# Optimization experiments

Hardware: AMD Instinct MI355X
Metric: run time of the kernel (lower is better)

Reference implementation:

```python
import jax, jax.numpy as jnp
import numpy as np

EMBED_DIM = 1024
NUM_HEADS = 16
HEAD_DIM = EMBED_DIM // NUM_HEADS
BATCH = 4
SEQ = 2048


def setup_inputs() -> dict:
    key = jax.random.key(0)
    ks = jax.random.split(key, 5)
    s_in = 1.0 / np.sqrt(EMBED_DIM)
    x = jax.random.normal(ks[0], (BATCH, SEQ, EMBED_DIM), dtype=jnp.float32)
    # torch nn.Linear params: weight [out, in], bias [out]
    qkv_w = jax.random.uniform(ks[1], (3 * EMBED_DIM, EMBED_DIM), jnp.float32, -s_in, s_in)
    qkv_b = jax.random.uniform(ks[2], (3 * EMBED_DIM,), jnp.float32, -s_in, s_in)
    out_w = jax.random.uniform(ks[3], (EMBED_DIM, EMBED_DIM), jnp.float32, -s_in, s_in)
    out_b = jax.random.uniform(ks[4], (EMBED_DIM,), jnp.float32, -s_in, s_in)
    return {"x": x, "qkv_w": qkv_w, "qkv_b": qkv_b, "out_w": out_w, "out_b": out_b}


def reference(x, qkv_w, qkv_b, out_w, out_b):
    B, S, E = x.shape
    qkv = x @ qkv_w.T + qkv_b                      # [B,S,3E]
    qkv = qkv.reshape(B, S, 3, NUM_HEADS, HEAD_DIM)
    qkv = jnp.transpose(qkv, (2, 0, 3, 1, 4))      # [3,B,H,S,D]
    q, k, v = qkv[0], qkv[1], qkv[2]
    scale = jnp.sqrt(jnp.float32(HEAD_DIM))
    scores = jnp.einsum('bhqd,bhkd->bhqk', q, k) / scale  # [B,H,S,S]
    attn = jax.nn.softmax(scores, axis=-1)
    out = jnp.einsum('bhqk,bhkd->bhqd', attn, v)   # [B,H,S,D]
    out = jnp.transpose(out, (0, 2, 1, 3)).reshape(B, S, E)
    return out @ out_w.T + out_b
```

## Files before the change

kernel.cpp:

```cpp
#include <hip/hip_runtime.h>
#include <hip/hip_bf16.h>

typedef _Float16 f16;
typedef __attribute__((ext_vector_type(8))) _Float16 f16x8;
typedef __attribute__((ext_vector_type(4))) _Float16 f16x4;
typedef __attribute__((ext_vector_type(4))) float f32x4;

#define MFMA16(a, b, c) __builtin_amdgcn_mfma_f32_16x16x32_f16(a, b, c, 0, 0, 0)
#define GLDS(src, dst) __builtin_amdgcn_global_load_lds( \
    (const __attribute__((address_space(1))) void*)(src), \
    (__attribute__((address_space(3))) void*)(dst), 16, 0, 0)

__device__ inline unsigned pkrtz(float a, float b) {
    __fp16 __attribute__((ext_vector_type(2))) r = __builtin_amdgcn_cvt_pkrtz(a, b);
    unsigned u; __builtin_memcpy(&u, &r, 4);
    return u;
}
__device__ inline void pl32swap(unsigned& a, unsigned& b) {
    asm volatile("v_permlane32_swap_b32 %0, %1" : "+v"(a), "+v"(b));
}
__device__ inline void pl16swap(unsigned& a, unsigned& b) {
    asm volatile("v_permlane16_swap_b32 %0, %1" : "+v"(a), "+v"(b));
}
__device__ inline float fexp2(float x) {
#if __has_builtin(__builtin_amdgcn_exp2f)
    return __builtin_amdgcn_exp2f(x);
#else
    return exp2f(x);
#endif
}

__global__ void cvt_all(const float4* __restrict__ x, const float4* __restrict__ qw,
                        const float4* __restrict__ ow,
                        f16x4* __restrict__ xo, f16x4* __restrict__ qwo,
                        f16x4* __restrict__ owo) {
    const int N1 = 2097152, N2 = 786432, N3 = 262144;
    int i = blockIdx.x * blockDim.x + threadIdx.x;
    int stride = gridDim.x * blockDim.x;
    for (; i < N1 + N2 + N3; i += stride) {
        const float4* src; f16x4* dst; int j;
        if (i < N1)            { src = x;  dst = xo;  j = i; }
        else if (i < N1 + N2)  { src = qw; dst = qwo; j = i - N1; }
        else                   { src = ow; dst = owo; j = i - N1 - N2; }
        float4 f = src[j];
        f16x4 h;
        h.x = (f16)f.x; h.y = (f16)f.y; h.z = (f16)f.z; h.w = (f16)f.w;
        dst[j] = h;
    }
}

__global__ __launch_bounds__(256, 2) void gemm_bt(
    const f16* __restrict__ A, const f16* __restrict__ Bw,
    const float* __restrict__ bias, int mode, int nbn, int chunk,
    f16* __restrict__ qo, f16* __restrict__ ko, f16* __restrict__ vo,
    float* __restrict__ outp)
{
    __shared__ __align__(16) f16 As[128 * 64];
    __shared__ __align__(16) f16 Bs[128 * 64];
    const int bid = blockIdx.x;
    const int vid = (bid & 7) * chunk + (bid >> 3);
    const int brow = (vid / nbn) * 128;
    const int bcol = (vid % nbn) * 128;
    const int tid = threadIdx.x;
    const int wave = tid >> 6, lane = tid & 63;
    const int wr = wave >> 1, wc = wave & 1;
    const int K = 1024;
    const f16* Ab = A + (size_t)brow * K;
    const f16* Bb = Bw + (size_t)bcol * K;

    const f32x4 fz = {0.0f, 0.0f, 0.0f, 0.0f};
    f32x4 acc[4][4];
#pragma unroll
    for (int m = 0; m < 4; ++m)
#pragma unroll
        for (int n = 0; n < 4; ++n) acc[m][n] = fz;

    const int lrow = lane >> 3;
    const int lcol = (lane & 7) * 8;
    const int cl = lane & 15, rg = lane >> 4;

    for (int k0 = 0; k0 < K; k0 += 64) {
        __syncthreads();
#pragma unroll
        for (int c = 0; c < 4; ++c) {
            const int ch = wave * 4 + c;
            GLDS(Ab + (size_t)(ch * 8 + lrow) * K + k0 + lcol, As + ch * 512);
            GLDS(Bb + (size_t)(ch * 8 + lrow) * K + k0 + lcol, Bs + ch * 512);
        }
        __syncthreads();
#pragma unroll
        for (int kk = 0; kk < 2; ++kk) {
            f16x8 af[4], bfr[4];
#pragma unroll
            for (int m = 0; m < 4; ++m)
                af[m] = *(const f16x8*)(As + (wr * 64 + m * 16 + cl) * 64 + kk * 32 + rg * 8);
#pragma unroll
            for (int n = 0; n < 4; ++n)
                bfr[n] = *(const f16x8*)(Bs + (wc * 64 + n * 16 + cl) * 64 + kk * 32 + rg * 8);
#pragma unroll
            for (int m = 0; m < 4; ++m)
#pragma unroll
                for (int n = 0; n < 4; ++n)
                    acc[m][n] = MFMA16(af[m], bfr[n], acc[m][n]);
        }
    }

    if (mode == 0) {
#pragma unroll
        for (int n = 0; n < 4; ++n) {
            int col = bcol + wc * 64 + n * 16 + cl;
            float bs = bias[col];
            int which = col >> 10;
            int h = (col & 1023) >> 6;
            int d = col & 63;
            if (which == 2) {
#pragma unroll
                for (int m = 0; m < 4; ++m) {
                    int row0 = brow + wr * 64 + m * 16 + rg * 4;
                    int bb = row0 >> 11, s0 = row0 & 2047;
                    f16x4 pk;
#pragma unroll
                    for (int r = 0; r < 4; ++r) pk[r] = (f16)(acc[m][n][r] + bs);
                    *(f16x4*)(vo + ((size_t)(bb * 16 + h) * 64 + d) * 2048 + s0) = pk;
                }
            } else {
                f16* dst = (which == 0) ? qo : ko;
                float scale = (which == 0) ? 0.125f * 1.44269504f : 1.0f;
#pragma unroll
                for (int m = 0; m < 4; ++m) {
#pragma unroll
                    for (int r = 0; r < 4; ++r) {
                        int row = brow + wr * 64 + m * 16 + rg * 4 + r;
                        int bb = row >> 11, s = row & 2047;
                        dst[((size_t)(bb * 16 + h) * 2048 + s) * 64 + d] =
                            (f16)((acc[m][n][r] + bs) * scale);
                    }
                }
            }
        }
    } else {
#pragma unroll
        for (int n = 0; n < 4; ++n) {
            int col = bcol + wc * 64 + n * 16 + cl;
            float bs = bias[col];
#pragma unroll
            for (int m = 0; m < 4; ++m)
#pragma unroll
                for (int r = 0; r < 4; ++r) {
                    int row = brow + wr * 64 + m * 16 + rg * 4 + r;
                    outp[(size_t)row * 1024 + col] = acc[m][n][r] + bs;
                }
        }
    }
}

__global__ __launch_bounds__(256, 3) void attn_fwd(
    const f16* __restrict__ Q, const f16* __restrict__ Kg,
    const f16* __restrict__ Vtg, f16* __restrict__ AO)
{
    const int bid = blockIdx.x;
    const int vid = (bid & 7) * 128 + (bid >> 3);
    const int qx = vid & 15;
    const int bh = vid >> 4;
    const int q0 = qx * 128;
    const int tid = threadIdx.x;
    const int wave = tid >> 6, lane = tid & 63;
    const int cl = lane & 15, rg = lane >> 4;
    const f16* Qh = Q + (size_t)bh * 2048 * 64;
    const f16* Kp = Kg + (size_t)bh * 2048 * 64;
    const f16* Vp = Vtg + (size_t)bh * 64 * 2048;

    __shared__ __align__(16) f16 Ks[2][64 * 64];
    __shared__ __align__(16) f16 Vs[2][64 * 64];

    f16x8 aq[2][2];
#pragma unroll
    for (int m = 0; m < 2; ++m) {
        const f16* qptr = Qh + (size_t)(q0 + wave * 32 + m * 16 + cl) * 64 + rg * 8;
        aq[m][0] = *(const f16x8*)(qptr);
        aq[m][1] = *(const f16x8*)(qptr + 32);
    }

    f16x8 ones8;
#pragma unroll
    for (int j = 0; j < 8; ++j) ones8[j] = (f16)1.0f;

    const int srow0 = tid >> 3;
    const int schunk = tid & 7;
    const int swz = cl & 7;

    const f32x4 fz = {0.0f, 0.0f, 0.0f, 0.0f};
    f32x4 oacc[2][4];
    f32x4 loacc[2];
#pragma unroll
    for (int m = 0; m < 2; ++m) {
        loacc[m] = fz;
#pragma unroll
        for (int da = 0; da < 4; ++da) oacc[m][da] = fz;
    }

#pragma unroll
    for (int c = 0; c < 2; ++c) {
        int row = c * 32 + srow0;
        int sc = (schunk ^ (row & 7)) * 8;
        GLDS(Kp + (size_t)row * 64 + sc,   &Ks[0][(c * 256 + wave * 64) * 8]);
        GLDS(Vp + (size_t)row * 2048 + sc, &Vs[0][(c * 256 + wave * 64) * 8]);
    }

    int cur = 0;
    for (int t = 0; t < 32; ++t) {
        if (t < 31) {
            const int kt = (t + 1) * 64;
#pragma unroll
            for (int c = 0; c < 2; ++c) {
                int row = c * 32 + srow0;
                int sc = (schunk ^ (row & 7)) * 8;
                GLDS(Kp + (size_t)(kt + row) * 64 + sc, &Ks[cur ^ 1][(c * 256 + wave * 64) * 8]);
                GLDS(Vp + (size_t)row * 2048 + kt + sc, &Vs[cur ^ 1][(c * 256 + wave * 64) * 8]);
            }
            asm volatile("s_waitcnt vmcnt(4)" ::: "memory");
        } else {
            asm volatile("s_waitcnt vmcnt(0)" ::: "memory");
        }
        __builtin_amdgcn_sched_barrier(0);
        __builtin_amdgcn_s_barrier();
        __builtin_amdgcn_sched_barrier(0);

        f32x4 sacc[2][4];
        __builtin_amdgcn_s_setprio(1);
#pragma unroll
        for (int fn = 0; fn < 4; ++fn) {
            f16x8 ak0 = *(const f16x8*)(
                &Ks[cur][(fn * 16 + cl) * 64 + (rg ^ swz) * 8]);
            f16x8 ak1 = *(const f16x8*)(
                &Ks[cur][(fn * 16 + cl) * 64 + ((4 | rg) ^ swz) * 8]);
            sacc[0][fn] = MFMA16(ak0, aq[0][0], fz);
            sacc[0][fn] = MFMA16(ak1, aq[0][1], sacc[0][fn]);
            sacc[1][fn] = MFMA16(ak0, aq[1][0], fz);
            sacc[1][fn] = MFMA16(ak1, aq[1][1], sacc[1][fn]);
        }
        __builtin_amdgcn_s_setprio(0);

        f16x8 pbv[2][2];
#pragma unroll
        for (int m = 0; m < 2; ++m) {
            unsigned X0[4], X1[4];
#pragma unroll
            for (int fn = 0; fn < 4; ++fn) {
                float p0 = fexp2(sacc[m][fn][0]);
                float p1 = fexp2(sacc[m][fn][1]);
                float p2 = fexp2(sacc[m][fn][2]);
                float p3 = fexp2(sacc[m][fn][3]);
                X0[fn] = pkrtz(p0, p1);
                X1[fn] = pkrtz(p2, p3);
            }
#pragma unroll
            for (int kk = 0; kk < 2; ++kk) {
                unsigned a0 = X0[2 * kk], b0 = X0[2 * kk + 1];
                unsigned a1 = X1[2 * kk], b1 = X1[2 * kk + 1];
                pl32swap(a0, b0); pl16swap(a0, b0);
                pl32swap(a1, b1); pl16swap(a1, b1);
                unsigned fr[4] = {a0, a1, b0, b1};
                __builtin_memcpy(&pbv[m][kk], fr, 16);
            }
        }

        __builtin_amdgcn_s_setprio(1);
#pragma unroll
        for (int kk = 0; kk < 2; ++kk) {
            loacc[0] = MFMA16(ones8, pbv[0][kk], loacc[0]);
            loacc[1] = MFMA16(ones8, pbv[1][kk], loacc[1]);
#pragma unroll
            for (int da = 0; da < 4; ++da) {
                f16x8 av = *(const f16x8*)(
                    &Vs[cur][(da * 16 + cl) * 64 + (((kk << 2) | rg) ^ swz) * 8]);
                oacc[0][da] = MFMA16(av, pbv[0][kk], oacc[0][da]);
                oacc[1][da] = MFMA16(av, pbv[1][kk], oacc[1][da]);
            }
        }
        __builtin_amdgcn_s_setprio(0);

        asm volatile("s_waitcnt lgkmcnt(0)" ::: "memory");
        __builtin_amdgcn_sched_barrier(0);
        __builtin_amdgcn_s_barrier();
        __builtin_amdgcn_sched_barrier(0);
        cur ^= 1;
    }

    const int bb = bh >> 4, h = bh & 15;
#pragma unroll
    for (int m = 0; m < 2; ++m) {
        float inv = 1.0f / loacc[m][0];
        int s = q0 + wave * 32 + m * 16 + cl;
        f16* op = AO + ((size_t)(bb * 2048 + s) * 16 + h) * 64;
#pragma unroll
        for (int da = 0; da < 4; ++da) {
            f16x4 ov;
#pragma unroll
            for (int r = 0; r < 4; ++r) ov[r] = (f16)(oacc[m][da][r] * inv);
            *(f16x4*)(op + da * 16 + rg * 4) = ov;
        }
    }
}

extern "C" void kernel_launch(void* const* d_in, const int* in_sizes, int n_in,
                              void* d_out, int out_size, void* d_ws, size_t ws_size,
                              hipStream_t stream) {
    const float* x     = (const float*)d_in[0];
    const float* qkv_w = (const float*)d_in[1];
    const float* qkv_b = (const float*)d_in[2];
    const float* out_w = (const float*)d_in[3];
    const float* out_b = (const float*)d_in[4];
    float* out = (float*)d_out;

    char* ws = (char*)d_ws;
    size_t off = 0;
    f16* x_h  = (f16*)(ws + off); off += 16777216;
    f16* qw_h = (f16*)(ws + off); off += 6291456;
    f16* ow_h = (f16*)(ws + off); off += 2097152;
    f16* Qb   = (f16*)(ws + off); off += 16777216;
    f16* Kb   = (f16*)(ws + off); off += 16777216;
    f16* Vb   = (f16*)(ws + off); off += 16777216;
    f16* AO   = (f16*)(ws + off); off += 16777216;

    cvt_all<<<2048, 256, 0, stream>>>((const float4*)x, (const float4*)qkv_w,
                                      (const float4*)out_w,
                                      (f16x4*)x_h, (f16x4*)qw_h, (f16x4*)ow_h);

    gemm_bt<<<1536, dim3(256), 0, stream>>>(x_h, qw_h, qkv_b, 0, 24, 192,
                                            Qb, Kb, Vb, nullptr);
    attn_fwd<<<1024, dim3(256), 0, stream>>>(Qb, Kb, Vb, AO);
    gemm_bt<<<512, dim3(256), 0, stream>>>(AO, ow_h, out_b, 1, 8, 64,
                                           nullptr, nullptr, nullptr, out);
}
```

Measured before the change: 189.2 us.

## Add 256x256 double-buffered QKV GEMM kernel with swizzled LDS and phased pipeline

Replaces the generic 128x128 QKV projection GEMM with a dedicated 256x256-tile kernel using 512 threads. It double-buffers LDS, XOR-swizzles the shared-memory layout, and interleaves global-to-LDS loads with MFMA phases under explicit waitcnt, barriers and setprio. The aim is more data reuse per tile and hiding of load latency. The output GEMM becomes its own specialised kernel. The cost is 128 KB of LDS per block and only 384 blocks, which lowers occupancy and risks tail imbalance across CUs.

```diff
diff --git a/kernel.cpp b/kernel.cpp
--- a/kernel.cpp
+++ b/kernel.cpp
@@ -49,18 +49,158 @@
     }
 }
 
-__global__ __launch_bounds__(256, 2) void gemm_bt(
+__global__ __launch_bounds__(512, 2) void gemm256_qkv(
     const f16* __restrict__ A, const f16* __restrict__ Bw,
-    const float* __restrict__ bias, int mode, int nbn, int chunk,
-    f16* __restrict__ qo, f16* __restrict__ ko, f16* __restrict__ vo,
-    float* __restrict__ outp)
+    const float* __restrict__ bias,
+    f16* __restrict__ qo, f16* __restrict__ ko, f16* __restrict__ vo)
+{
+    __shared__ __align__(16) f16 As[2][16384];
+    __shared__ __align__(16) f16 Bs[2][16384];
+    const int tid = threadIdx.x;
+    const int wave = tid >> 6, lane = tid & 63;
+    const int wr = wave >> 2, wc = wave & 3;
+    const int bid = blockIdx.x;
+    const int vid = (bid & 7) * 48 + (bid >> 3);
+    const int brow = (vid / 12) * 256;
+    const int bcol = (vid % 12) * 256;
+    const f16* Ab = A + (size_t)brow * 1024;
+    const f16* Bb = Bw + (size_t)bcol * 1024;
+
+    const int cl = lane & 15, rg = lane >> 4;
+    const int swz = cl & 7;
+    const int strow = tid >> 3;
+    const int ssc = ((tid & 7) ^ (strow & 7)) * 8;
+
+#define STG_A(db, s, kcol) GLDS(Ab + (size_t)((s) * 64 + strow) * 1024 + (kcol) + ssc, \
+                                &As[db][(s) * 4096 + wave * 512])
+#define STG_B(db, s, kcol) GLDS(Bb + (size_t)((s) * 64 + strow) * 1024 + (kcol) + ssc, \
+                                &Bs[db][(s) * 4096 + wave * 512])
+
+    const f32x4 fz = {0.0f, 0.0f, 0.0f, 0.0f};
+    f32x4 acc[8][4];
+#pragma unroll
+    for (int m = 0; m < 8; ++m)
+#pragma unroll
+        for (int n = 0; n < 4; ++n) acc[m][n] = fz;
+    f16x8 bf[4][2];
+
+#pragma unroll
+    for (int s = 0; s < 4; ++s) STG_A(0, s, 0);
+#pragma unroll
+    for (int s = 0; s < 4; ++s) STG_B(0, s, 0);
+#pragma unroll
+    for (int s = 0; s < 4; ++s) STG_B(1, s, 64);
+    STG_A(1, 0, 64); STG_A(1, 2, 64);
+    asm volatile("s_waitcnt vmcnt(6)" ::: "memory");
+    __builtin_amdgcn_sched_barrier(0);
+    __builtin_amdgcn_s_barrier();
+    __builtin_amdgcn_sched_barrier(0);
+
+#define PHASE(BUF, Q, BW, ...)                                                   \
+    do {                                                                         \
+        f16x8 af[2][2];                                                          \
+        _Pragma("unroll")                                                        \
+        for (int mi = 0; mi < 2; ++mi)                                           \
+            _Pragma("unroll")                                                    \
+            for (int kk = 0; kk < 2; ++kk)                                       \
+                af[mi][kk] = *(const f16x8*)(&As[BUF][(wr * 2 + ((Q) >> 1)) * 4096 \
+                    + (((Q) & 1) * 32 + mi * 16 + cl) * 64                       \
+                    + (((kk << 2) | rg) ^ swz) * 8]);                            \
+        if ((Q) == 0) {                                                          \
+            _Pragma("unroll")                                                    \
+            for (int n = 0; n < 4; ++n)                                          \
+                _Pragma("unroll")                                                \
+                for (int kk = 0; kk < 2; ++kk)                                   \
+                    bf[n][kk] = *(const f16x8*)(&Bs[BUF][wc * 4096               \
+                        + (n * 16 + cl) * 64 + (((kk << 2) | rg) ^ swz) * 8]);   \
+        }                                                                        \
+        __VA_ARGS__;                                                             \
+        if ((Q) == 0) asm volatile("s_waitcnt lgkmcnt(8)" ::: "memory");         \
+        __builtin_amdgcn_sched_barrier(0);                                       \
+        __builtin_amdgcn_s_barrier();                                            \
+        asm volatile("s_waitcnt lgkmcnt(0)" ::: "memory");                       \
+        __builtin_amdgcn_sched_barrier(0);                                       \
+        __builtin_amdgcn_s_setprio(1);                                           \
+        _Pragma("unroll")                                                        \
+        for (int n = 0; n < 4; ++n) {                                            \
+            acc[(Q) * 2 + 0][n] = MFMA16(af[0][0], bf[n][0], acc[(Q) * 2 + 0][n]); \
+            acc[(Q) * 2 + 0][n] = MFMA16(af[0][1], bf[n][1], acc[(Q) * 2 + 0][n]); \
+            acc[(Q) * 2 + 1][n] = MFMA16(af[1][0], bf[n][0], acc[(Q) * 2 + 1][n]); \
+            acc[(Q) * 2 + 1][n] = MFMA16(af[1][1], bf[n][1], acc[(Q) * 2 + 1][n]); \
+        }                                                                        \
+        __builtin_amdgcn_s_setprio(0);                                           \
+        if ((BW) == 6)      asm volatile("s_waitcnt vmcnt(6)" ::: "memory");     \
+        else if ((BW) == 0) asm volatile("s_waitcnt vmcnt(0)" ::: "memory");     \
+        __builtin_amdgcn_sched_barrier(0);                                       \
+        __builtin_amdgcn_s_barrier();                                            \
+        __builtin_amdgcn_sched_barrier(0);                                       \
+    } while (0)
+
+    for (int i = 0; i < 8; ++i) {
+        const int K0 = 2 * i, K1 = 2 * i + 1;
+        const int kA1 = (K0 + 1) * 64;
+        const int kN0 = (K0 + 2) * 64;
+        const int kA2 = (K1 + 1) * 64;
+        const int kN1 = (K1 + 2) * 64;
+        PHASE(0, 0, -1, { STG_A(1, 1, kA1); STG_A(1, 3, kA1); });
+        PHASE(0, 1, -1, if (K0 <= 13) { STG_B(0, 0, kN0); STG_B(0, 1, kN0); });
+        PHASE(0, 2, -1, if (K0 <= 13) { STG_B(0, 2, kN0); STG_B(0, 3, kN0); });
+        PHASE(0, 3, (K0 <= 13 ? 6 : 0),
+                        if (K0 <= 13) { STG_A(0, 0, kN0); STG_A(0, 2, kN0); });
+        PHASE(1, 0, -1, if (K1 <= 14) { STG_A(0, 1, kA2); STG_A(0, 3, kA2); });
+        PHASE(1, 1, -1, if (K1 <= 13) { STG_B(1, 0, kN1); STG_B(1, 1, kN1); });
+        PHASE(1, 2, -1, if (K1 <= 13) { STG_B(1, 2, kN1); STG_B(1, 3, kN1); });
+        PHASE(1, 3, (K1 <= 13 ? 6 : (K1 == 15 ? -1 : 0)),
+                        if (K1 <= 13) { STG_A(1, 0, kN1); STG_A(1, 2, kN1); });
+    }
+#undef PHASE
+#undef STG_A
+#undef STG_B
+
+#pragma unroll
+    for (int n = 0; n < 4; ++n) {
+        int col = bcol + wc * 64 + n * 16 + cl;
+        float bs = bias[col];
+        int which = col >> 10;
+        int h = (col & 1023) >> 6;
+        int d = col & 63;
+        if (which == 2) {
+#pragma unroll
+            for (int m = 0; m < 8; ++m) {
+                int row0 = brow + wr * 128 + m * 16 + rg * 4;
+                int bb = row0 >> 11, s0 = row0 & 2047;
+                f16x4 pk;
+#pragma unroll
+                for (int r = 0; r < 4; ++r) pk[r] = (f16)(acc[m][n][r] + bs);
+                *(f16x4*)(vo + ((size_t)(bb * 16 + h) * 64 + d) * 2048 + s0) = pk;
+            }
+        } else {
+            f16* dst = (which == 0) ? qo : ko;
+            float scale = (which == 0) ? 0.125f * 1.44269504f : 1.0f;
+#pragma unroll
+            for (int m = 0; m < 8; ++m) {
+#pragma unroll
+                for (int r = 0; r < 4; ++r) {
+                    int row = brow + wr * 128 + m * 16 + rg * 4 + r;
+                    int bb = row >> 11, s = row & 2047;
+                    dst[((size_t)(bb * 16 + h) * 2048 + s) * 64 + d] =
+                        (f16)((acc[m][n][r] + bs) * scale);
+                }
+            }
+        }
+    }
+}
+
+__global__ __launch_bounds__(256, 2) void gemm_out(
+    const f16* __restrict__ A, const f16* __restrict__ Bw,
+    const float* __restrict__ bias, float* __restrict__ outp)
 {
     __shared__ __align__(16) f16 As[128 * 64];
     __shared__ __align__(16) f16 Bs[128 * 64];
     const int bid = blockIdx.x;
-    const int vid = (bid & 7) * chunk + (bid >> 3);
-    const int brow = (vid / nbn) * 128;
-    const int bcol = (vid % nbn) * 128;
+    const int vid = (bid & 7) * 64 + (bid >> 3);
+    const int brow = (vid / 8) * 128;
+    const int bcol = (vid % 8) * 128;
     const int tid = threadIdx.x;
     const int wave = tid >> 6, lane = tid & 63;
     const int wr = wave >> 1, wc = wave & 1;
@@ -104,53 +244,17 @@
                     acc[m][n] = MFMA16(af[m], bfr[n], acc[m][n]);
         }
     }
-
-    if (mode == 0) {
-#pragma unroll
-        for (int n = 0; n < 4; ++n) {
-            int col = bcol + wc * 64 + n * 16 + cl;
-            float bs = bias[col];
-            int which = col >> 10;
-            int h = (col & 1023) >> 6;
-            int d = col & 63;
-            if (which == 2) {
-#pragma unroll
-                for (int m = 0; m < 4; ++m) {
-                    int row0 = brow + wr * 64 + m * 16 + rg * 4;
-                    int bb = row0 >> 11, s0 = row0 & 2047;
-                    f16x4 pk;
-#pragma unroll
-                    for (int r = 0; r < 4; ++r) pk[r] = (f16)(acc[m][n][r] + bs);
-                    *(f16x4*)(vo + ((size_t)(bb * 16 + h) * 64 + d) * 2048 + s0) = pk;
-                }
-            } else {
-                f16* dst = (which == 0) ? qo : ko;
-                float scale = (which == 0) ? 0.125f * 1.44269504f : 1.0f;
-#pragma unroll
-                for (int m = 0; m < 4; ++m) {
-#pragma unroll
-                    for (int r = 0; r < 4; ++r) {
-                        int row = brow + wr * 64 + m * 16 + rg * 4 + r;
-                        int bb = row >> 11, s = row & 2047;
-                        dst[((size_t)(bb * 16 + h) * 2048 + s) * 64 + d] =
-                            (f16)((acc[m][n][r] + bs) * scale);
-                    }
-                }
-            }
-        }
-    } else {
-#pragma unroll
-        for (int n = 0; n < 4; ++n) {
-            int col = bcol + wc * 64 + n * 16 + cl;
-            float bs = bias[col];
-#pragma unroll
-            for (int m = 0; m < 4; ++m)
-#pragma unroll
-                for (int r = 0; r < 4; ++r) {
-                    int row = brow + wr * 64 + m * 16 + rg * 4 + r;
-                    outp[(size_t)row * 1024 + col] = acc[m][n][r] + bs;
-                }
-        }
+#pragma unroll
+    for (int n = 0; n < 4; ++n) {
+        int col = bcol + wc * 64 + n * 16 + cl;
+        float bs = bias[col];
+#pragma unroll
+        for (int m = 0; m < 4; ++m)
+#pragma unroll
+            for (int r = 0; r < 4; ++r) {
+                int row = brow + wr * 64 + m * 16 + rg * 4 + r;
+                outp[(size_t)row * 1024 + col] = acc[m][n][r] + bs;
+            }
     }
 }
 
@@ -327,9 +431,7 @@
                                       (const float4*)out_w,
                                       (f16x4*)x_h, (f16x4*)qw_h, (f16x4*)ow_h);
 
-    gemm_bt<<<1536, dim3(256), 0, stream>>>(x_h, qw_h, qkv_b, 0, 24, 192,
-                                            Qb, Kb, Vb, nullptr);
+    gemm256_qkv<<<384, dim3(512), 0, stream>>>(x_h, qw_h, qkv_b, Qb, Kb, Vb);
     attn_fwd<<<1024, dim3(256), 0, stream>>>(Qb, Kb, Vb, AO);
-    gemm_bt<<<512, dim3(256), 0, stream>>>(AO, ow_h, out_b, 1, 8, 64,
-                                           nullptr, nullptr, nullptr, out);
-}
+    gemm_out<<<512, dim3(256), 0, stream>>>(AO, ow_h, out_b, out);
+}
```

New measurement: 203.9 us. 7.8% more time.
